# Kernel tuning notes

Measured on AMD Instinct MI355X. Metric: run time of the kernel, lower is better.

The kernel has to match this reference:

```python
import jax, jax.numpy as jnp
import numpy as np

B, S, D = 4, 2048, 1024
H, HD = 8, 128
EPS = 1e-5
NEG = -1e30


def layernorm(x, w, b):
    mu = jnp.mean(x, axis=-1, keepdims=True)
    var = jnp.mean(jnp.square(x - mu), axis=-1, keepdims=True)
    return (x - mu) * jax.lax.rsqrt(var + EPS) * w + b


def rmsnorm(x, w):
    ms = jnp.mean(jnp.square(x), axis=-1, keepdims=True)
    return x * jax.lax.rsqrt(ms + EPS) * w


def setup_inputs() -> dict:
    key = jax.random.key(0)
    ks = jax.random.split(key, 8)
    scale = 0.02
    return {
        "layer_input": jax.random.normal(ks[0], (B, S, D), jnp.float32),
        "positions": jnp.broadcast_to(jnp.arange(S, dtype=jnp.int32), (B, S)),
        "ln_in_w": jnp.ones((D,), jnp.float32),
        "ln_in_b": jnp.zeros((D,), jnp.float32),
        "W_uvqk": jax.random.normal(ks[1], (D, 4 * H * HD), jnp.float32) * scale,
        "b_uvqk": jax.random.normal(ks[2], (4 * H * HD,), jnp.float32) * scale,
        "ln_out_w": jnp.ones((H * HD,), jnp.float32),
        "ln_out_b": jnp.zeros((H * HD,), jnp.float32),
        "W_proj": jax.random.normal(ks[3], (H * HD, D), jnp.float32) * scale,
        "rms_w": jnp.ones((D,), jnp.float32),
        "W1": jax.random.normal(ks[4], (D, 2 * D), jnp.float32) * scale,
        "W2": jax.random.normal(ks[5], (D, D), jnp.float32) * scale,
    }


def reference(layer_input, positions, ln_in_w, ln_in_b, W_uvqk, b_uvqk,
              ln_out_w, ln_out_b, W_proj, rms_w, W1, W2):
    # --- HSTU attention block ---
    normed = layernorm(layer_input, ln_in_w, ln_in_b)              # [B,S,D]
    mixed = jax.nn.silu(normed @ W_uvqk + b_uvqk)                  # [B,S,4*H*HD]
    user, value, query, key = jnp.split(mixed, 4, axis=-1)
    q = query.reshape(B, S, H, HD)
    k = key.reshape(B, S, H, HD)
    v = value.reshape(B, S, H, HD)
    alpha = 1.0 / np.sqrt(HD).astype(np.float32)
    scores = jnp.einsum("bqhd,bkhd->bhqk", q, k) * alpha           # [B,H,S,S]
    causal = jnp.tril(jnp.ones((S, S), bool))
    scores = jnp.where(causal, scores, NEG)
    probs = jax.nn.softmax(scores, axis=-1)
    attn = jnp.einsum("bhqk,bkhd->bqhd", probs, v).reshape(B, S, H * HD)
    # output norm * user gate, then projection
    parallel = user * layernorm(attn, ln_out_w, ln_out_b)          # [B,S,H*HD]
    layer_output = parallel @ W_proj                               # [B,S,D]
    # --- residual add + RMSNorm + SwiGLU FFN ---
    summed = layer_output + layer_input
    ffn_in = rmsnorm(summed, rms_w)
    h = ffn_in @ W1                                                # [B,S,2D]
    a, b = jnp.split(h, 2, axis=-1)                                # a <- w3, b <- w1
    ffn_out = (jax.nn.silu(a) * b) @ W2
    return ffn_out + layer_output
```

## Files before the change

kernel.cpp:

```cpp
#include <hip/hip_runtime.h>
#include <stdint.h>

typedef unsigned short u16;
typedef __bf16 bf16x8_t __attribute__((ext_vector_type(8)));
typedef float f32x4_t __attribute__((ext_vector_type(4)));

#define D_MODEL 1024
#define SEQ 2048
#define BATCH 4
#define NROWS (BATCH * SEQ)
#define HDIM 128

constexpr int EPI_SILU_BIAS = 0;
constexpr int EPI_F32 = 1;
constexpr int EPI_BF16 = 2;
constexpr int EPI_ADD_F32 = 3;

__device__ __forceinline__ float bf2f(u16 u) {
  union { unsigned int i; float f; } v; v.i = ((unsigned int)u) << 16; return v.f;
}
__device__ __forceinline__ u16 f2bf(float f) {
  union { float f; unsigned int i; } v; v.f = f;
  unsigned int r = (v.i + 0x7FFFu + ((v.i >> 16) & 1u)) >> 16;
  return (u16)r;
}
__device__ __forceinline__ float silu_f(float x) { return x / (1.0f + __expf(-x)); }

__device__ __forceinline__ void load_lds16(const void* g, void* l) {
  auto gp = (const __attribute__((address_space(1))) char*)(uintptr_t)g;
  auto lp = (__attribute__((address_space(3))) char*)(uint32_t)(uintptr_t)l;
  __builtin_amdgcn_global_load_lds(gp, lp, 16, 0, 0);
}

__device__ __forceinline__ void block_sum2(float& a, float& b, float* sm) {
  #pragma unroll
  for (int off = 32; off > 0; off >>= 1) {
    a += __shfl_xor(a, off, 64);
    b += __shfl_xor(b, off, 64);
  }
  const int w = threadIdx.x >> 6;
  if ((threadIdx.x & 63) == 0) { sm[w] = a; sm[4 + w] = b; }
  __syncthreads();
  a = sm[0] + sm[1] + sm[2] + sm[3];
  b = sm[4] + sm[5] + sm[6] + sm[7];
}

__global__ __launch_bounds__(256)
void k_wconv(const float* __restrict__ W, u16* __restrict__ Wt, int K, int N) {
  __shared__ float tile[32][33];
  const int n0 = blockIdx.x * 32, k0 = blockIdx.y * 32;
  const int tx = threadIdx.x & 31, ty = threadIdx.x >> 5;
  #pragma unroll
  for (int i = 0; i < 4; i++)
    tile[ty + 8 * i][tx] = W[(size_t)(k0 + ty + 8 * i) * N + n0 + tx];
  __syncthreads();
  #pragma unroll
  for (int i = 0; i < 4; i++)
    Wt[(size_t)(n0 + ty + 8 * i) * K + k0 + tx] = f2bf(tile[tx][ty + 8 * i]);
}

__global__ __launch_bounds__(256)
void k_ln_in(const float* __restrict__ X, const float* __restrict__ w,
             const float* __restrict__ b, u16* __restrict__ Y) {
  __shared__ float sm[8];
  const int row = blockIdx.x, t = threadIdx.x;
  const float4 v = ((const float4*)(X + (size_t)row * D_MODEL))[t];
  float s = v.x + v.y + v.z + v.w;
  float ss = v.x * v.x + v.y * v.y + v.z * v.z + v.w * v.w;
  block_sum2(s, ss, sm);
  const float mu = s * (1.0f / D_MODEL);
  const float var = ss * (1.0f / D_MODEL) - mu * mu;
  const float rs = rsqrtf(var + 1e-5f);
  const float4 wv = ((const float4*)w)[t];
  const float4 bv = ((const float4*)b)[t];
  ushort4 o;
  o.x = f2bf((v.x - mu) * rs * wv.x + bv.x);
  o.y = f2bf((v.y - mu) * rs * wv.y + bv.y);
  o.z = f2bf((v.z - mu) * rs * wv.z + bv.z);
  o.w = f2bf((v.w - mu) * rs * wv.w + bv.w);
  ((ushort4*)(Y + (size_t)row * D_MODEL))[t] = o;
}

__global__ __launch_bounds__(256)
void k_gated(const u16* __restrict__ attn, const u16* __restrict__ mixed,
             const float* __restrict__ w, const float* __restrict__ b,
             u16* __restrict__ out) {
  __shared__ float sm[8];
  const int row = blockIdx.x, t = threadIdx.x;
  const ushort4 av = ((const ushort4*)(attn + (size_t)row * D_MODEL))[t];
  const float x0 = bf2f(av.x), x1 = bf2f(av.y), x2 = bf2f(av.z), x3 = bf2f(av.w);
  float s = x0 + x1 + x2 + x3;
  float ss = x0 * x0 + x1 * x1 + x2 * x2 + x3 * x3;
  block_sum2(s, ss, sm);
  const float mu = s * (1.0f / D_MODEL);
  const float rs = rsqrtf(ss * (1.0f / D_MODEL) - mu * mu + 1e-5f);
  const ushort4 uv = ((const ushort4*)(mixed + (size_t)row * 4096))[t];
  const float4 wv = ((const float4*)w)[t];
  const float4 bv = ((const float4*)b)[t];
  ushort4 o;
  o.x = f2bf(bf2f(uv.x) * ((x0 - mu) * rs * wv.x + bv.x));
  o.y = f2bf(bf2f(uv.y) * ((x1 - mu) * rs * wv.y + bv.y));
  o.z = f2bf(bf2f(uv.z) * ((x2 - mu) * rs * wv.z + bv.z));
  o.w = f2bf(bf2f(uv.w) * ((x3 - mu) * rs * wv.w + bv.w));
  ((ushort4*)(out + (size_t)row * D_MODEL))[t] = o;
}

__global__ __launch_bounds__(256)
void k_rms(const float* __restrict__ lo, const float* __restrict__ li,
           const float* __restrict__ w, u16* __restrict__ out) {
  __shared__ float sm[8];
  const int row = blockIdx.x, t = threadIdx.x;
  const float4 a = ((const float4*)(lo + (size_t)row * D_MODEL))[t];
  const float4 bq = ((const float4*)(li + (size_t)row * D_MODEL))[t];
  const float x0 = a.x + bq.x, x1 = a.y + bq.y, x2 = a.z + bq.z, x3 = a.w + bq.w;
  float ss = x0 * x0 + x1 * x1 + x2 * x2 + x3 * x3, dummy = 0.f;
  block_sum2(ss, dummy, sm);
  const float rs = rsqrtf(ss * (1.0f / D_MODEL) + 1e-5f);
  const float4 wv = ((const float4*)w)[t];
  ushort4 o;
  o.x = f2bf(x0 * rs * wv.x);
  o.y = f2bf(x1 * rs * wv.y);
  o.z = f2bf(x2 * rs * wv.z);
  o.w = f2bf(x3 * rs * wv.w);
  ((ushort4*)(out + (size_t)row * D_MODEL))[t] = o;
}

__global__ __launch_bounds__(256)
void k_silumul(const u16* __restrict__ h, u16* __restrict__ g) {
  const int row = blockIdx.x, t = threadIdx.x;
  const ushort4 a = ((const ushort4*)(h + (size_t)row * 2048))[t];
  const ushort4 b = ((const ushort4*)(h + (size_t)row * 2048 + 1024))[t];
  ushort4 o;
  o.x = f2bf(silu_f(bf2f(a.x)) * bf2f(b.x));
  o.y = f2bf(silu_f(bf2f(a.y)) * bf2f(b.y));
  o.z = f2bf(silu_f(bf2f(a.z)) * bf2f(b.z));
  o.w = f2bf(silu_f(bf2f(a.w)) * bf2f(b.w));
  ((ushort4*)(g + (size_t)row * D_MODEL))[t] = o;
}

template <int EPI>
__global__ __launch_bounds__(256, 2)
void k_gemm(const u16* __restrict__ A, const u16* __restrict__ Bt,
            void* __restrict__ Cout, const float* __restrict__ bias,
            const float* __restrict__ addsrc, int M, int N, int K) {
  __shared__ u16 As[128 * 64];
  __shared__ u16 Bs[128 * 64];
  const int t = threadIdx.x, lane = t & 63, w = t >> 6;
  const int l15 = lane & 15, l4 = lane >> 4;
  const int wr = w >> 1, wc = w & 1;
  const int m0 = blockIdx.x * 128, n0 = blockIdx.y * 128;
  const int lr = lane >> 3, lc = lane & 7;
  const int swz = (lc ^ lr) * 8;

  f32x4_t acc[4][4];
  #pragma unroll
  for (int mi = 0; mi < 4; mi++)
    #pragma unroll
    for (int ni = 0; ni < 4; ni++) {
      acc[mi][ni][0] = 0.f; acc[mi][ni][1] = 0.f; acc[mi][ni][2] = 0.f; acc[mi][ni][3] = 0.f;
    }

  const u16* Ab = A + (size_t)m0 * K + swz;
  const u16* Bb = Bt + (size_t)n0 * K + swz;

  for (int kt = 0; kt < K; kt += 64) {
    #pragma unroll
    for (int j = 0; j < 4; j++) {
      const size_t rr = (size_t)((w * 4 + j) * 8 + lr);
      load_lds16(Ab + rr * K + kt, &As[(w * 4 + j) * 512]);
      load_lds16(Bb + rr * K + kt, &Bs[(w * 4 + j) * 512]);
    }
    __syncthreads();
    #pragma unroll
    for (int kk = 0; kk < 2; kk++) {
      bf16x8_t af[4], bf[4];
      #pragma unroll
      for (int mi = 0; mi < 4; mi++) {
        const int row = wr * 64 + mi * 16 + l15;
        const int cph = (kk * 4 + l4) ^ (row & 7);
        af[mi] = *(const bf16x8_t*)&As[row * 64 + cph * 8];
      }
      #pragma unroll
      for (int ni = 0; ni < 4; ni++) {
        const int row = wc * 64 + ni * 16 + l15;
        const int cph = (kk * 4 + l4) ^ (row & 7);
        bf[ni] = *(const bf16x8_t*)&Bs[row * 64 + cph * 8];
      }
      #pragma unroll
      for (int mi = 0; mi < 4; mi++)
        #pragma unroll
        for (int ni = 0; ni < 4; ni++)
          acc[mi][ni] = __builtin_amdgcn_mfma_f32_16x16x32_bf16(af[mi], bf[ni], acc[mi][ni], 0, 0, 0);
    }
    __syncthreads();
  }

  #pragma unroll
  for (int mi = 0; mi < 4; mi++) {
    #pragma unroll
    for (int ni = 0; ni < 4; ni++) {
      const int col = n0 + wc * 64 + ni * 16 + l15;
      float bv = 0.f;
      if constexpr (EPI == EPI_SILU_BIAS) bv = bias[col];
      #pragma unroll
      for (int r = 0; r < 4; r++) {
        const size_t row = (size_t)(m0 + wr * 64 + mi * 16 + l4 * 4 + r);
        float v = acc[mi][ni][r];
        if constexpr (EPI == EPI_SILU_BIAS) {
          v += bv;
          ((u16*)Cout)[row * N + col] = f2bf(silu_f(v));
        } else if constexpr (EPI == EPI_BF16) {
          ((u16*)Cout)[row * N + col] = f2bf(v);
        } else if constexpr (EPI == EPI_F32) {
          ((float*)Cout)[row * N + col] = v;
        } else {
          ((float*)Cout)[row * N + col] = v + addsrc[row * N + col];
        }
      }
    }
  }
}

__global__ __launch_bounds__(256)
void k_qkvprep(const u16* __restrict__ mixed, u16* __restrict__ Kc, u16* __restrict__ Vtc) {
  __shared__ u16 Vl[64 * 132];
  const int kt = blockIdx.x, bh = blockIdx.y, bI = bh >> 3, h = bh & 7;
  const int kb = kt * 64, t = threadIdx.x;
  const u16* base = mixed + (size_t)bI * SEQ * 4096;
  const int kcol = 3 * D_MODEL + h * HDIM;
  const int vcol = 1 * D_MODEL + h * HDIM;
  #pragma unroll
  for (int j = 0; j < 4; j++) {
    const int n = j * 256 + t, kr = n >> 4, c8 = n & 15;
    const uint4 kv = *(const uint4*)(base + (size_t)(kb + kr) * 4096 + kcol + c8 * 8);
    *(uint4*)(Kc + ((size_t)bh * SEQ + kb + kr) * 128 + c8 * 8) = kv;
    const uint4 vv = *(const uint4*)(base + (size_t)(kb + kr) * 4096 + vcol + c8 * 8);
    *(uint4*)&Vl[kr * 132 + c8 * 8] = vv;
  }
  __syncthreads();
  u16* vt = Vtc + ((size_t)bh * 32 + kt) * 8192;
  #pragma unroll
  for (int j = 0; j < 4; j++) {
    const int n = j * 256 + t, d = n >> 3, g8 = n & 7;
    u16 tmp[8];
    #pragma unroll
    for (int i = 0; i < 8; i++) tmp[i] = Vl[(g8 * 8 + i) * 132 + d];
    *(uint4*)(vt + d * 64 + g8 * 8) = *(const uint4*)tmp;
  }
}

__global__ __launch_bounds__(256, 2)
void k_attn(const u16* __restrict__ mixed, const u16* __restrict__ Kc,
            const u16* __restrict__ Vtc, u16* __restrict__ attnb) {
  __shared__ u16 Ks[64 * 128];
  __shared__ u16 Vts[128 * 64];
  __shared__ u16 Ps[4 * 16 * 64];
  const int t = threadIdx.x, lane = t & 63, w = t >> 6;
  const int l15 = lane & 15, l4 = lane >> 4;
  const int bh = blockIdx.y, bI = bh >> 3, h = bh & 7;
  const int qt = 15 - blockIdx.x;
  const int qb = qt * 128;
  const u16* base = mixed + (size_t)bI * SEQ * 4096;
  const int qcol = 2 * D_MODEL + h * HDIM;
  const int qrow0 = qb + w * 32;
  const u16* Kh = Kc + (size_t)bh * SEQ * 128;
  const u16* Vh = Vtc + (size_t)bh * 32 * 8192;

  const int nk = lane;

  bf16x8_t qf[2][4];
  #pragma unroll
  for (int mi = 0; mi < 2; mi++) {
    const u16* qp = base + (size_t)(qrow0 + mi * 16 + l15) * 4096 + qcol + l4 * 8;
    #pragma unroll
    for (int ks = 0; ks < 4; ks++) qf[mi][ks] = *(const bf16x8_t*)(qp + ks * 32);
  }

  f32x4_t o[2][8];
  #pragma unroll
  for (int mi = 0; mi < 2; mi++)
    #pragma unroll
    for (int df = 0; df < 8; df++) { o[mi][df][0] = 0.f; o[mi][df][1] = 0.f; o[mi][df][2] = 0.f; o[mi][df][3] = 0.f; }
  float mrun[2][4], lrun[2][4];
  #pragma unroll
  for (int mi = 0; mi < 2; mi++)
    #pragma unroll
    for (int r = 0; r < 4; r++) { mrun[mi][r] = -1e30f; lrun[mi][r] = 0.f; }

  const float alpha = 0.08838834764831845f;
  const int nkt = qb / 64 + 2;

  auto stage = [&](int tile) {
    const u16* Kt = Kh + (size_t)(tile * 64) * 128;
    const u16* Vt = Vh + (size_t)tile * 8192;
    #pragma unroll
    for (int j = 0; j < 4; j++) {
      const int slot = j * 4 + w;
      const int kr = slot * 4 + (nk >> 4), gk = nk & 15;
      load_lds16(Kt + kr * 128 + ((gk ^ (kr & 7)) * 8), &Ks[slot * 512]);
      const int d = slot * 8 + (nk >> 3), gv = nk & 7;
      load_lds16(Vt + d * 64 + ((gv ^ (d & 7) ^ ((d >> 3) & 7)) * 8), &Vts[slot * 512]);
    }
  };

  for (int it = 0; it < nkt; it++) {
    const int kb = it * 64;
    stage(it);
    __syncthreads();

    const bool active = (kb <= qrow0 + 31);
    const bool needmask = (kb + 63 > qrow0);
    if (active) {
      f32x4_t s[2][4];
      #pragma unroll
      for (int mi = 0; mi < 2; mi++)
        #pragma unroll
        for (int ni = 0; ni < 4; ni++) { s[mi][ni][0] = 0.f; s[mi][ni][1] = 0.f; s[mi][ni][2] = 0.f; s[mi][ni][3] = 0.f; }
      #pragma unroll
      for (int ks = 0; ks < 4; ks++) {
        bf16x8_t kf[4];
        #pragma unroll
        for (int ni = 0; ni < 4; ni++) {
          const int key = ni * 16 + l15;
          const int cph = (ks * 4 + l4) ^ (key & 7);
          kf[ni] = *(const bf16x8_t*)&Ks[key * 128 + cph * 8];
        }
        #pragma unroll
        for (int mi = 0; mi < 2; mi++)
          #pragma unroll
          for (int ni = 0; ni < 4; ni++)
            s[mi][ni] = __builtin_amdgcn_mfma_f32_16x16x32_bf16(qf[mi][ks], kf[ni], s[mi][ni], 0, 0, 0);
      }
      #pragma unroll
      for (int mi = 0; mi < 2; mi++) {
        #pragma unroll
        for (int r = 0; r < 4; r++) {
          const int qr = qrow0 + mi * 16 + l4 * 4 + r;
          float mx = -1e30f;
          #pragma unroll
          for (int ni = 0; ni < 4; ni++) {
            float v = s[mi][ni][r] * alpha;
            if (needmask) {
              const int key = kb + ni * 16 + l15;
              if (key > qr) v = -1e30f;
            }
            s[mi][ni][r] = v;
            mx = fmaxf(mx, v);
          }
          #pragma unroll
          for (int off = 1; off < 16; off <<= 1) mx = fmaxf(mx, __shfl_xor(mx, off, 64));
          const float mnew = fmaxf(mrun[mi][r], mx);
          const float fsc = __expf(mrun[mi][r] - mnew);
          mrun[mi][r] = mnew;
          lrun[mi][r] *= fsc;
          #pragma unroll
          for (int df = 0; df < 8; df++) o[mi][df][r] *= fsc;
          float ls = 0.f;
          #pragma unroll
          for (int ni = 0; ni < 4; ni++) {
            const float p = __expf(s[mi][ni][r] - mnew);
            s[mi][ni][r] = p;
            ls += p;
          }
          #pragma unroll
          for (int off = 1; off < 16; off <<= 1) ls += __shfl_xor(ls, off, 64);
          lrun[mi][r] += ls;
        }
        #pragma unroll
        for (int ni = 0; ni < 4; ni++)
          #pragma unroll
          for (int r = 0; r < 4; r++) {
            const int pr = l4 * 4 + r;
            const int pc = ni * 16 + l15;
            Ps[w * 1024 + pr * 64 + (((pc >> 3) ^ (pr & 7)) * 8) + (pc & 7)] = f2bf(s[mi][ni][r]);
          }
        #pragma unroll
        for (int ks2 = 0; ks2 < 2; ks2++) {
          bf16x8_t pa;
          {
            const int pr = l15;
            const int cph = (ks2 * 4 + l4) ^ (pr & 7);
            pa = *(const bf16x8_t*)&Ps[w * 1024 + pr * 64 + cph * 8];
          }
          #pragma unroll
          for (int df = 0; df < 8; df++) {
            const int d = df * 16 + l15;
            const int cph = (ks2 * 4 + l4) ^ (d & 7) ^ ((d >> 3) & 7);
            const bf16x8_t vb = *(const bf16x8_t*)&Vts[d * 64 + cph * 8];
            o[mi][df] = __builtin_amdgcn_mfma_f32_16x16x32_bf16(pa, vb, o[mi][df], 0, 0, 0);
          }
        }
      }
    }
    __syncthreads();
  }

  #pragma unroll
  for (int mi = 0; mi < 2; mi++) {
    #pragma unroll
    for (int r = 0; r < 4; r++) {
      const float inv = 1.0f / lrun[mi][r];
      const size_t row = (size_t)bI * SEQ + qrow0 + mi * 16 + l4 * 4 + r;
      #pragma unroll
      for (int df = 0; df < 8; df++)
        attnb[row * D_MODEL + h * HDIM + df * 16 + l15] = f2bf(o[mi][df][r] * inv);
    }
  }
}

extern "C" void kernel_launch(void* const* d_in, const int* in_sizes, int n_in,
                              void* d_out, int out_size, void* d_ws, size_t ws_size,
                              hipStream_t stream) {
  (void)in_sizes; (void)n_in; (void)out_size; (void)ws_size;
  const float* layer_input = (const float*)d_in[0];
  const float* ln_in_w  = (const float*)d_in[2];
  const float* ln_in_b  = (const float*)d_in[3];
  const float* W_uvqk   = (const float*)d_in[4];
  const float* b_uvqk   = (const float*)d_in[5];
  const float* ln_out_w = (const float*)d_in[6];
  const float* ln_out_b = (const float*)d_in[7];
  const float* W_proj   = (const float*)d_in[8];
  const float* rms_w    = (const float*)d_in[9];
  const float* W1       = (const float*)d_in[10];
  const float* W2       = (const float*)d_in[11];
  float* out = (float*)d_out;

  char* ws = (char*)d_ws;
  u16* buf0    = (u16*)(ws);
  u16* mixed   = (u16*)(ws + ((size_t)16 << 20));
  u16* attnb   = (u16*)(ws + ((size_t)80 << 20));
  float* lout  = (float*)(ws + ((size_t)96 << 20));
  u16* Kc      = (u16*)(ws + ((size_t)96 << 20));
  u16* Vtc     = (u16*)(ws + ((size_t)112 << 20));
  u16* wt_uvqk = (u16*)(ws + ((size_t)128 << 20));
  u16* wt_proj = (u16*)(ws + ((size_t)136 << 20));
  u16* wt_1    = (u16*)(ws + ((size_t)138 << 20));
  u16* wt_2    = (u16*)(ws + ((size_t)142 << 20));

  k_wconv<<<dim3(128, 32), 256, 0, stream>>>(W_uvqk, wt_uvqk, 1024, 4096);
  k_wconv<<<dim3(32, 32), 256, 0, stream>>>(W_proj, wt_proj, 1024, 1024);
  k_wconv<<<dim3(64, 32), 256, 0, stream>>>(W1, wt_1, 1024, 2048);
  k_wconv<<<dim3(32, 32), 256, 0, stream>>>(W2, wt_2, 1024, 1024);

  k_ln_in<<<NROWS, 256, 0, stream>>>(layer_input, ln_in_w, ln_in_b, buf0);
  k_gemm<EPI_SILU_BIAS><<<dim3(64, 32), 256, 0, stream>>>(buf0, wt_uvqk, mixed, b_uvqk, nullptr, NROWS, 4096, 1024);
  k_qkvprep<<<dim3(32, 32), 256, 0, stream>>>(mixed, Kc, Vtc);
  k_attn<<<dim3(16, 32), 256, 0, stream>>>(mixed, Kc, Vtc, attnb);
  k_gated<<<NROWS, 256, 0, stream>>>(attnb, mixed, ln_out_w, ln_out_b, buf0);
  k_gemm<EPI_F32><<<dim3(64, 8), 256, 0, stream>>>(buf0, wt_proj, lout, nullptr, nullptr, NROWS, 1024, 1024);
  k_rms<<<NROWS, 256, 0, stream>>>(lout, layer_input, rms_w, buf0);
  k_gemm<EPI_BF16><<<dim3(64, 16), 256, 0, stream>>>(buf0, wt_1, mixed, nullptr, nullptr, NROWS, 2048, 1024);
  k_silumul<<<NROWS, 256, 0, stream>>>(mixed, buf0);
  k_gemm<EPI_ADD_F32><<<dim3(64, 8), 256, 0, stream>>>(buf0, wt_2, out, nullptr, lout, NROWS, 1024, 1024);
}
```

Baseline: 403.3 us.

## Prefetch next K/V tile into registers, lazily rescale softmax, reswizzle P LDS

The attention loop now loads the next K/V tile from global memory into registers while computing on the current tile, then writes those registers to LDS after a barrier. This replaces direct global-to-LDS loads followed by an immediate sync, with the aim of hiding global load latency. The online softmax skips the running-max update and rescaling of the output accumulators when the new max stays within a threshold of the old one. The P scratch swizzle also gains an extra XOR term to reduce LDS bank conflicts. The costs are an extra barrier per iteration and higher register pressure from the staged tiles.

```diff
diff --git a/kernel.cpp b/kernel.cpp
--- a/kernel.cpp
+++ b/kernel.cpp
@@ -290,23 +290,38 @@
   const float alpha = 0.08838834764831845f;
   const int nkt = qb / 64 + 2;
 
-  auto stage = [&](int tile) {
+  const int krA = (nk >> 4), gk = nk & 15;
+  const int dA  = (nk >> 3), gv = nk & 7;
+
+  uint4 kreg[4], vreg[4];
+  auto loadregs = [&](int tile) {
     const u16* Kt = Kh + (size_t)(tile * 64) * 128;
     const u16* Vt = Vh + (size_t)tile * 8192;
     #pragma unroll
     for (int j = 0; j < 4; j++) {
       const int slot = j * 4 + w;
-      const int kr = slot * 4 + (nk >> 4), gk = nk & 15;
-      load_lds16(Kt + kr * 128 + ((gk ^ (kr & 7)) * 8), &Ks[slot * 512]);
-      const int d = slot * 8 + (nk >> 3), gv = nk & 7;
-      load_lds16(Vt + d * 64 + ((gv ^ (d & 7) ^ ((d >> 3) & 7)) * 8), &Vts[slot * 512]);
+      const int kr = slot * 4 + krA;
+      kreg[j] = *(const uint4*)(Kt + kr * 128 + ((gk ^ (kr & 7)) * 8));
+      const int d = slot * 8 + dA;
+      vreg[j] = *(const uint4*)(Vt + d * 64 + ((gv ^ (d & 7) ^ ((d >> 3) & 7)) * 8));
     }
   };
+  auto writeregs = [&]() {
+    #pragma unroll
+    for (int j = 0; j < 4; j++) {
+      const int slot = j * 4 + w;
+      *(uint4*)&Ks[slot * 512 + lane * 8] = kreg[j];
+      *(uint4*)&Vts[slot * 512 + lane * 8] = vreg[j];
+    }
+  };
+
+  loadregs(0);
+  writeregs();
+  __syncthreads();
 
   for (int it = 0; it < nkt; it++) {
     const int kb = it * 64;
-    stage(it);
-    __syncthreads();
+    if (it + 1 < nkt) loadregs(it + 1);
 
     const bool active = (kb <= qrow0 + 31);
     const bool needmask = (kb + 63 > qrow0);
@@ -349,16 +364,18 @@
           }
           #pragma unroll
           for (int off = 1; off < 16; off <<= 1) mx = fmaxf(mx, __shfl_xor(mx, off, 64));
-          const float mnew = fmaxf(mrun[mi][r], mx);
-          const float fsc = __expf(mrun[mi][r] - mnew);
-          mrun[mi][r] = mnew;
-          lrun[mi][r] *= fsc;
-          #pragma unroll
-          for (int df = 0; df < 8; df++) o[mi][df][r] *= fsc;
+          if (!__all(mx <= mrun[mi][r] + 8.0f)) {
+            const float mnew = fmaxf(mrun[mi][r], mx);
+            const float fsc = __expf(mrun[mi][r] - mnew);
+            mrun[mi][r] = mnew;
+            lrun[mi][r] *= fsc;
+            #pragma unroll
+            for (int df = 0; df < 8; df++) o[mi][df][r] *= fsc;
+          }
           float ls = 0.f;
           #pragma unroll
           for (int ni = 0; ni < 4; ni++) {
-            const float p = __expf(s[mi][ni][r] - mnew);
+            const float p = __expf(s[mi][ni][r] - mrun[mi][r]);
             s[mi][ni][r] = p;
             ls += p;
           }
@@ -372,14 +389,15 @@
           for (int r = 0; r < 4; r++) {
             const int pr = l4 * 4 + r;
             const int pc = ni * 16 + l15;
-            Ps[w * 1024 + pr * 64 + (((pc >> 3) ^ (pr & 7)) * 8) + (pc & 7)] = f2bf(s[mi][ni][r]);
+            const int ch = ((pc >> 3) ^ (pr & 7) ^ ((pr & 8) >> 1));
+            Ps[w * 1024 + pr * 64 + ch * 8 + (pc & 7)] = f2bf(s[mi][ni][r]);
           }
         #pragma unroll
         for (int ks2 = 0; ks2 < 2; ks2++) {
           bf16x8_t pa;
           {
             const int pr = l15;
-            const int cph = (ks2 * 4 + l4) ^ (pr & 7);
+            const int cph = (ks2 * 4 + l4) ^ (pr & 7) ^ ((pr & 8) >> 1);
             pa = *(const bf16x8_t*)&Ps[w * 1024 + pr * 64 + cph * 8];
           }
           #pragma unroll
@@ -392,6 +410,8 @@
         }
       }
     }
+    __syncthreads();
+    if (it + 1 < nkt) writeregs();
     __syncthreads();
   }
 
```

Result: slower. 427.3 us (+5.9%).

## Split long causal attention query tiles across two blocks with combine pass

Applied to the files above, without the earlier changes.

Query tiles in the upper half of the sequence are split into two blocks, each processing half the key range. Partial outputs and running max/sum go to scratch space carved out of the output buffer. A new combine kernel merges them with log-sum-exp rescaling. This is meant to balance work across the causal triangle and add blocks for better occupancy, at the cost of an extra launch, extra memory traffic, and bf16 rounding of the unnormalized partials.

```diff
diff --git a/kernel.cpp b/kernel.cpp
--- a/kernel.cpp
+++ b/kernel.cpp
@@ -251,15 +251,24 @@
 
 __global__ __launch_bounds__(256, 2)
 void k_attn(const u16* __restrict__ mixed, const u16* __restrict__ Kc,
-            const u16* __restrict__ Vtc, u16* __restrict__ attnb) {
+            const u16* __restrict__ Vtc, u16* __restrict__ attnb,
+            u16* __restrict__ o_part, float* __restrict__ ml) {
   __shared__ u16 Ks[64 * 128];
   __shared__ u16 Vts[128 * 64];
   __shared__ u16 Ps[4 * 16 * 64];
   const int t = threadIdx.x, lane = t & 63, w = t >> 6;
   const int l15 = lane & 15, l4 = lane >> 4;
   const int bh = blockIdx.y, bI = bh >> 3, h = bh & 7;
-  const int qt = 15 - blockIdx.x;
+  const int ci = blockIdx.x;
+  int qt, ch;
+  if (ci < 16) { qt = 15 - (ci >> 1); ch = ci & 1; }
+  else { qt = 23 - ci; ch = 0; }
+  const bool split = (qt >= 8);
   const int qb = qt * 128;
+  const int nt_all = 2 * qt + 2;
+  const int t0 = (split && ch == 1) ? (qt + 1) : 0;
+  const int t1 = (split && ch == 0) ? (qt + 1) : nt_all;
+
   const u16* base = mixed + (size_t)bI * SEQ * 4096;
   const int qcol = 2 * D_MODEL + h * HDIM;
   const int qrow0 = qb + w * 32;
@@ -288,7 +297,6 @@
     for (int r = 0; r < 4; r++) { mrun[mi][r] = -1e30f; lrun[mi][r] = 0.f; }
 
   const float alpha = 0.08838834764831845f;
-  const int nkt = qb / 64 + 2;
 
   auto stage = [&](int tile) {
     const u16* Kt = Kh + (size_t)(tile * 64) * 128;
@@ -303,7 +311,7 @@
     }
   };
 
-  for (int it = 0; it < nkt; it++) {
+  for (int it = t0; it < t1; it++) {
     const int kb = it * 64;
     stage(it);
     __syncthreads();
@@ -395,16 +403,71 @@
     __syncthreads();
   }
 
-  #pragma unroll
-  for (int mi = 0; mi < 2; mi++) {
-    #pragma unroll
-    for (int r = 0; r < 4; r++) {
-      const float inv = 1.0f / lrun[mi][r];
-      const size_t row = (size_t)bI * SEQ + qrow0 + mi * 16 + l4 * 4 + r;
-      #pragma unroll
-      for (int df = 0; df < 8; df++)
-        attnb[row * D_MODEL + h * HDIM + df * 16 + l15] = f2bf(o[mi][df][r] * inv);
-    }
+  if (!split) {
+    #pragma unroll
+    for (int mi = 0; mi < 2; mi++) {
+      #pragma unroll
+      for (int r = 0; r < 4; r++) {
+        const float inv = 1.0f / lrun[mi][r];
+        const size_t row = (size_t)bI * SEQ + qrow0 + mi * 16 + l4 * 4 + r;
+        #pragma unroll
+        for (int df = 0; df < 8; df++)
+          attnb[row * D_MODEL + h * HDIM + df * 16 + l15] = f2bf(o[mi][df][r] * inv);
+      }
+    }
+  } else {
+    const int sl = bh * 8 + (qt - 8);
+    #pragma unroll
+    for (int mi = 0; mi < 2; mi++) {
+      #pragma unroll
+      for (int r = 0; r < 4; r++) {
+        const int pr = w * 32 + mi * 16 + l4 * 4 + r;
+        if (l15 == 0) {
+          ml[sl * 512 + ch * 256 + pr] = mrun[mi][r];
+          ml[sl * 512 + ch * 256 + 128 + pr] = lrun[mi][r];
+        }
+        if (ch == 0) {
+          const size_t row = (size_t)bI * SEQ + qb + pr;
+          #pragma unroll
+          for (int df = 0; df < 8; df++)
+            attnb[row * D_MODEL + h * HDIM + df * 16 + l15] = f2bf(o[mi][df][r]);
+        } else {
+          #pragma unroll
+          for (int df = 0; df < 8; df++)
+            o_part[(size_t)sl * 16384 + pr * 128 + df * 16 + l15] = f2bf(o[mi][df][r]);
+        }
+      }
+    }
+  }
+}
+
+__global__ __launch_bounds__(256)
+void k_combine(const u16* __restrict__ o_part, const float* __restrict__ ml,
+               u16* __restrict__ attnb) {
+  const int qti = blockIdx.x, bh = blockIdx.y;
+  const int bI = bh >> 3, h = bh & 7;
+  const int t = threadIdx.x;
+  const int pr = t >> 1, half = t & 1;
+  const int sl = bh * 8 + qti;
+  const float m0 = ml[sl * 512 + pr];
+  const float l0 = ml[sl * 512 + 128 + pr];
+  const float m1 = ml[sl * 512 + 256 + pr];
+  const float l1 = ml[sl * 512 + 384 + pr];
+  const float M = fmaxf(m0, m1);
+  const float w0 = __expf(m0 - M), w1 = __expf(m1 - M);
+  const float inv = 1.0f / (w0 * l0 + w1 * l1);
+  const float c0 = w0 * inv, c1 = w1 * inv;
+  const size_t row = (size_t)bI * SEQ + (8 + qti) * 128 + pr;
+  u16* ap = attnb + row * D_MODEL + h * HDIM + half * 64;
+  const u16* pp = o_part + (size_t)sl * 16384 + pr * 128 + half * 64;
+  #pragma unroll
+  for (int j = 0; j < 8; j++) {
+    u16 a[8], b[8], c[8];
+    *(uint4*)a = ((const uint4*)ap)[j];
+    *(uint4*)b = ((const uint4*)pp)[j];
+    #pragma unroll
+    for (int i = 0; i < 8; i++) c[i] = f2bf(c0 * bf2f(a[i]) + c1 * bf2f(b[i]));
+    ((uint4*)ap)[j] = *(const uint4*)c;
   }
 }
 
@@ -436,6 +499,8 @@
   u16* wt_proj = (u16*)(ws + ((size_t)136 << 20));
   u16* wt_1    = (u16*)(ws + ((size_t)138 << 20));
   u16* wt_2    = (u16*)(ws + ((size_t)142 << 20));
+  u16* o_part  = (u16*)d_out;
+  float* ml    = (float*)((char*)d_out + ((size_t)20 << 20));
 
   k_wconv<<<dim3(128, 32), 256, 0, stream>>>(W_uvqk, wt_uvqk, 1024, 4096);
   k_wconv<<<dim3(32, 32), 256, 0, stream>>>(W_proj, wt_proj, 1024, 1024);
@@ -445,7 +510,8 @@
   k_ln_in<<<NROWS, 256, 0, stream>>>(layer_input, ln_in_w, ln_in_b, buf0);
   k_gemm<EPI_SILU_BIAS><<<dim3(64, 32), 256, 0, stream>>>(buf0, wt_uvqk, mixed, b_uvqk, nullptr, NROWS, 4096, 1024);
   k_qkvprep<<<dim3(32, 32), 256, 0, stream>>>(mixed, Kc, Vtc);
-  k_attn<<<dim3(16, 32), 256, 0, stream>>>(mixed, Kc, Vtc, attnb);
+  k_attn<<<dim3(24, 32), 256, 0, stream>>>(mixed, Kc, Vtc, attnb, o_part, ml);
+  k_combine<<<dim3(8, 32), 256, 0, stream>>>(o_part, ml, attnb);
   k_gated<<<NROWS, 256, 0, stream>>>(attnb, mixed, ln_out_w, ln_out_b, buf0);
   k_gemm<EPI_F32><<<dim3(64, 8), 256, 0, stream>>>(buf0, wt_proj, lout, nullptr, nullptr, NROWS, 1024, 1024);
   k_rms<<<NROWS, 256, 0, stream>>>(lout, layer_input, rms_w, buf0);
```

New measurement: 405.1 us. Within noise of the previous version (+0.4%).
